# Performance work log

Hardware: AMD Instinct MI355X
Metric: run time of the kernel (lower is better)

Reference implementation:

```python
import jax, jax.numpy as jnp
import numpy as np

N_NODES = 50000
N_EDGES = 800000
ENT_DIM = 128
REL_DIM = 128
NUM_REL = 200  # relation table has 2*NUM_REL rows (forward + inverse)


def setup_inputs() -> dict:
    key = jax.random.key(0)
    ks = jax.random.split(key, 16)
    inp = {
        'src': jax.random.randint(ks[0], (N_EDGES,), 0, N_NODES),
        'dst': jax.random.randint(ks[1], (N_EDGES,), 0, N_NODES),
        'etypes': jax.random.randint(ks[2], (N_EDGES,), 0, 2 * NUM_REL),
        'ent_emb': jax.random.normal(ks[3], (N_NODES, ENT_DIM), jnp.float32),
        'rel_emb': jax.random.normal(ks[4], (2 * NUM_REL, REL_DIM), jnp.float32),
        'W_O_w': jax.random.normal(ks[5], (ENT_DIM, REL_DIM + ENT_DIM), jnp.float32) * 0.05,
        'W_O_b': jax.random.normal(ks[6], (ENT_DIM,), jnp.float32) * 0.05,
        'W_I_w': jax.random.normal(ks[7], (ENT_DIM, REL_DIM + ENT_DIM), jnp.float32) * 0.05,
        'W_I_b': jax.random.normal(ks[8], (ENT_DIM,), jnp.float32) * 0.05,
        'W_S_w': jax.random.normal(ks[9], (ENT_DIM, ENT_DIM), jnp.float32) * 0.05,
        'W_S_b': jax.random.normal(ks[10], (ENT_DIM,), jnp.float32) * 0.05,
        'W_R_w': jax.random.normal(ks[11], (REL_DIM, REL_DIM), jnp.float32) * 0.05,
        'W_R_b': jax.random.normal(ks[12], (REL_DIM,), jnp.float32) * 0.05,
    }
    return inp


def reference(src, dst, etypes, ent_emb, rel_emb,
              W_O_w, W_O_b, W_I_w, W_I_b, W_S_w, W_S_b, W_R_w, W_R_b):
    # msg_func: per-edge gather of relation emb and source node emb, concat,
    # then route through W_O (type < num_rel) or W_I (type >= num_rel).
    comp_h = jnp.concatenate([rel_emb[etypes], ent_emb[src]], axis=-1)  # [E, rel+ent]
    msg_o = comp_h @ W_O_w.T + W_O_b  # [E, ent]
    msg_i = comp_h @ W_I_w.T + W_I_b
    non_inv = (etypes < NUM_REL)[:, None]
    msg = jnp.where(non_inv, msg_o, msg_i)
    # fn.mean('msg','h_agg'): scatter-mean into destination nodes (0 if no in-edges)
    agg_sum = jax.ops.segment_sum(msg, dst, num_segments=N_NODES)
    deg = jax.ops.segment_sum(jnp.ones((msg.shape[0],), msg.dtype), dst,
                              num_segments=N_NODES)
    h_agg = agg_sum / jnp.maximum(deg, 1.0)[:, None]
    # apply_node_func (act is None -> identity)
    ent_new = ent_emb @ W_S_w.T + W_S_b + h_agg
    # edge_update
    rel_new = rel_emb @ W_R_w.T + W_R_b
    return ent_new, rel_new
```

## Files before the change

kernel.cpp:

```cpp
#include <hip/hip_runtime.h>
#include <hip/hip_bf16.h>

#define N_NODES 50000
#define N_EDGES 800000
#define DIM 128
#define NUM_REL 200
#define NREL2 (2 * NUM_REL)
#define NROWG (N_NODES / 16)
#define NBLK_G ((NROWG + 3) / 4)
#define NODES_PER_XCD (N_NODES / 8)
#define CAP 64
#define ZROW (2 * N_NODES)
#define ZREL NREL2
#define ZPAY (ZROW | (ZREL << 17))

typedef __bf16 bf16x8 __attribute__((ext_vector_type(8)));
typedef float f32x4 __attribute__((ext_vector_type(4)));

__global__ void __launch_bounds__(256)
prep_kernel(const float* __restrict__ W_O_w, const float* __restrict__ W_I_w,
            const float* __restrict__ W_S_w,
            __bf16* __restrict__ WTh, __bf16* __restrict__ WTl,
            int* __restrict__ counts, __bf16* __restrict__ EEb,
            __bf16* __restrict__ Rb) {
    const int idx = blockIdx.x * 256 + threadIdx.x;
    if (idx < 384 * DIM) {
        const int j = idx >> 7;
        const int k = idx & 127;
        float v;
        if (j < 128) v = W_O_w[j * (2 * DIM) + DIM + k];
        else if (j < 256) v = W_I_w[(j - 128) * (2 * DIM) + DIM + k];
        else v = W_S_w[(j - 256) * DIM + k];
        const __bf16 h = (__bf16)v;
        WTh[idx] = h;
        WTl[idx] = (__bf16)(v - (float)h);
    }
    if (idx < N_NODES) counts[idx] = 0;
    if (idx < DIM) {
        EEb[(size_t)ZROW * DIM + idx] = (__bf16)0.f;
        Rb[(size_t)ZREL * DIM + idx] = (__bf16)0.f;
    }
}

__global__ void rel_tables_kernel(const float* __restrict__ rel_emb,
                                  const float* __restrict__ W_O_w,
                                  const float* __restrict__ W_O_b,
                                  const float* __restrict__ W_I_w,
                                  const float* __restrict__ W_I_b,
                                  const float* __restrict__ W_R_w,
                                  const float* __restrict__ W_R_b,
                                  __bf16* __restrict__ Rb,
                                  float* __restrict__ rel_new) {
    __shared__ float row[DIM];
    const int t = blockIdx.x;
    const int j = threadIdx.x;
    row[j] = rel_emb[t * DIM + j];
    __syncthreads();

    const bool fwd = (t < NUM_REL);
    const float* __restrict__ wSel = (fwd ? W_O_w : W_I_w) + j * (2 * DIM);
    const float* __restrict__ wR = W_R_w + j * DIM;

    float aSel = 0.f, aR = 0.f;
#pragma unroll 8
    for (int k = 0; k < DIM; ++k) {
        const float e = row[k];
        aSel += e * wSel[k];
        aR += e * wR[k];
    }
    Rb[t * DIM + j] = (__bf16)(aSel + (fwd ? W_O_b[j] : W_I_b[j]));
    rel_new[t * DIM + j] = aR + W_R_b[j];
}

#define REP4(F) F(0) F(1) F(2) F(3)

__global__ void __launch_bounds__(256, 1)
mfma_gemm_kernel(const float* __restrict__ ent,
                 const __bf16* __restrict__ WTh, const __bf16* __restrict__ WTl,
                 const float* __restrict__ W_S_b,
                 __bf16* __restrict__ EEb, float* __restrict__ ent_S) {
    __shared__ __bf16 LBh[2][16 * 64 * 8];
    __shared__ __bf16 LBl[2][16 * 64 * 8];

    const int tid = threadIdx.x;
    const int wv = tid >> 6;
    const int rg = blockIdx.x * 4 + wv;
    const bool valid = (rg < NROWG);
    const int rgc = valid ? rg : (NROWG - 1);
    const int l = tid & 63;
    const int r16 = l & 15;
    const int kg = l >> 4;

    const float* __restrict__ aptr = ent + (size_t)(rgc * 16 + r16) * DIM + kg * 8;
#define ADECL(ks)                                                              \
    bf16x8 ah##ks, al##ks;                                                     \
    {                                                                          \
        const float4 v0 = *(const float4*)(aptr + (ks) * 32);                  \
        const float4 v1 = *(const float4*)(aptr + (ks) * 32 + 4);              \
        const float xs[8] = {v0.x, v0.y, v0.z, v0.w, v1.x, v1.y, v1.z, v1.w};  \
        _Pragma("unroll") for (int i = 0; i < 8; ++i) {                        \
            const __bf16 h = (__bf16)xs[i];                                    \
            ah##ks[i] = h;                                                     \
            al##ks[i] = (__bf16)(xs[i] - (float)h);                            \
        }                                                                      \
    }
    REP4(ADECL)
#undef ADECL

    const int orow = rgc * 16 + kg * 4;

#pragma unroll
    for (int i = 0; i < 4; ++i) {
        const int sks = i * 4 + wv;
        const int s = sks >> 2;
        const int ks = sks & 3;
        const size_t soff = (size_t)(s * 16 + r16) * DIM + ks * 32 + kg * 8;
        const int g = i * 256 + tid;
        *(bf16x8*)(&LBh[0][g * 8]) = *(const bf16x8*)(WTh + soff);
        *(bf16x8*)(&LBl[0][g * 8]) = *(const bf16x8*)(WTl + soff);
    }

#pragma unroll 1
    for (int cb = 0; cb < 6; ++cb) {
        __syncthreads();
        const int cur = cb & 1;
        const int nxt = cur ^ 1;

        bf16x8 ph0, ph1, ph2, ph3, pl0, pl1, pl2, pl3;
        if (cb < 5) {
            const int cbn = cb + 1;
#define PRE(i)                                                                 \
            {                                                                  \
                const int sks = (i) * 4 + wv;                                  \
                const int s = sks >> 2;                                        \
                const int ks = sks & 3;                                        \
                const size_t soff =                                            \
                    (size_t)(cbn * 64 + s * 16 + r16) * DIM + ks * 32 + kg * 8;\
                ph##i = *(const bf16x8*)(WTh + soff);                          \
                pl##i = *(const bf16x8*)(WTl + soff);                          \
            }
            PRE(0) PRE(1) PRE(2) PRE(3)
#undef PRE
        }

        f32x4 p0 = {0.f, 0.f, 0.f, 0.f}, q0 = {0.f, 0.f, 0.f, 0.f};
        f32x4 p1 = {0.f, 0.f, 0.f, 0.f}, q1 = {0.f, 0.f, 0.f, 0.f};
        f32x4 p2 = {0.f, 0.f, 0.f, 0.f}, q2 = {0.f, 0.f, 0.f, 0.f};
        f32x4 p3 = {0.f, 0.f, 0.f, 0.f}, q3 = {0.f, 0.f, 0.f, 0.f};

#define KS(ks)                                                                 \
    {                                                                          \
        const bf16x8 bh0 = *(const bf16x8*)(&LBh[cur][((0 * 4 + (ks)) * 64 + l) * 8]); \
        const bf16x8 bh1 = *(const bf16x8*)(&LBh[cur][((1 * 4 + (ks)) * 64 + l) * 8]); \
        const bf16x8 bh2 = *(const bf16x8*)(&LBh[cur][((2 * 4 + (ks)) * 64 + l) * 8]); \
        const bf16x8 bh3 = *(const bf16x8*)(&LBh[cur][((3 * 4 + (ks)) * 64 + l) * 8]); \
        const bf16x8 bl0 = *(const bf16x8*)(&LBl[cur][((0 * 4 + (ks)) * 64 + l) * 8]); \
        const bf16x8 bl1 = *(const bf16x8*)(&LBl[cur][((1 * 4 + (ks)) * 64 + l) * 8]); \
        const bf16x8 bl2 = *(const bf16x8*)(&LBl[cur][((2 * 4 + (ks)) * 64 + l) * 8]); \
        const bf16x8 bl3 = *(const bf16x8*)(&LBl[cur][((3 * 4 + (ks)) * 64 + l) * 8]); \
        p0 = __builtin_amdgcn_mfma_f32_16x16x32_bf16(ah##ks, bh0, p0, 0, 0, 0); \
        p1 = __builtin_amdgcn_mfma_f32_16x16x32_bf16(ah##ks, bh1, p1, 0, 0, 0); \
        p2 = __builtin_amdgcn_mfma_f32_16x16x32_bf16(ah##ks, bh2, p2, 0, 0, 0); \
        p3 = __builtin_amdgcn_mfma_f32_16x16x32_bf16(ah##ks, bh3, p3, 0, 0, 0); \
        q0 = __builtin_amdgcn_mfma_f32_16x16x32_bf16(al##ks, bh0, q0, 0, 0, 0); \
        q1 = __builtin_amdgcn_mfma_f32_16x16x32_bf16(al##ks, bh1, q1, 0, 0, 0); \
        q2 = __builtin_amdgcn_mfma_f32_16x16x32_bf16(al##ks, bh2, q2, 0, 0, 0); \
        q3 = __builtin_amdgcn_mfma_f32_16x16x32_bf16(al##ks, bh3, q3, 0, 0, 0); \
        q0 = __builtin_amdgcn_mfma_f32_16x16x32_bf16(ah##ks, bl0, q0, 0, 0, 0); \
        q1 = __builtin_amdgcn_mfma_f32_16x16x32_bf16(ah##ks, bl1, q1, 0, 0, 0); \
        q2 = __builtin_amdgcn_mfma_f32_16x16x32_bf16(ah##ks, bl2, q2, 0, 0, 0); \
        q3 = __builtin_amdgcn_mfma_f32_16x16x32_bf16(ah##ks, bl3, q3, 0, 0, 0); \
    }
        REP4(KS)
#undef KS

        if (cb < 5) {
#define WRT(i)                                                                 \
            {                                                                  \
                const int g = (i) * 256 + tid;                                 \
                *(bf16x8*)(&LBh[nxt][g * 8]) = ph##i;                          \
                *(bf16x8*)(&LBl[nxt][g * 8]) = pl##i;                          \
            }
            WRT(0) WRT(1) WRT(2) WRT(3)
#undef WRT
        }

        if (valid) {
            const int colb = (cb & 1) * 64;
            if (cb < 4) {
                __bf16* __restrict__ obb =
                    EEb + ((cb < 2) ? 0 : (size_t)N_NODES * DIM);
#define ST(s, P, Q)                                                            \
                {                                                              \
                    const int col = colb + (s) * 16 + r16;                     \
                    const f32x4 a = P + Q;                                     \
                    obb[(size_t)(orow + 0) * DIM + col] = (__bf16)a[0];        \
                    obb[(size_t)(orow + 1) * DIM + col] = (__bf16)a[1];        \
                    obb[(size_t)(orow + 2) * DIM + col] = (__bf16)a[2];        \
                    obb[(size_t)(orow + 3) * DIM + col] = (__bf16)a[3];        \
                }
                ST(0, p0, q0) ST(1, p1, q1) ST(2, p2, q2) ST(3, p3, q3)
#undef ST
            } else {
#define ST(s, P, Q)                                                            \
                {                                                              \
                    const int col = colb + (s) * 16 + r16;                     \
                    const float bs = W_S_b[col];                               \
                    const f32x4 a = P + Q;                                     \
                    ent_S[(size_t)(orow + 0) * DIM + col] = a[0] + bs;         \
                    ent_S[(size_t)(orow + 1) * DIM + col] = a[1] + bs;         \
                    ent_S[(size_t)(orow + 2) * DIM + col] = a[2] + bs;         \
                    ent_S[(size_t)(orow + 3) * DIM + col] = a[3] + bs;         \
                }
                ST(0, p0, q0) ST(1, p1, q1) ST(2, p2, q2) ST(3, p3, q3)
#undef ST
            }
        }
    }
}

__global__ void __launch_bounds__(256)
fill_kernel(const int* __restrict__ src, const int* __restrict__ dst,
            const int* __restrict__ et, int* __restrict__ counts,
            int* __restrict__ sp) {
    const int b = blockIdx.x;
    const int r = b & 7;
    const int e = (b >> 3) * 256 + threadIdx.x;
    const int d = dst[e];
    if ((unsigned)(d - r * NODES_PER_XCD) < (unsigned)NODES_PER_XCD) {
        const int t = et[e];
        const int row = src[e] + ((t < NUM_REL) ? 0 : N_NODES);
        const int pos = atomicAdd(&counts[d], 1);
        if (pos < CAP) sp[(d << 6) + pos] = row | (t << 17);
    }
}

__global__ void __launch_bounds__(256)
gather_kernel(const int* __restrict__ counts, const int* __restrict__ sp,
              const __bf16* __restrict__ EEb, const __bf16* __restrict__ Rb,
              const float* __restrict__ ent_S, float* __restrict__ out_ent) {
    const int node = blockIdx.x * 4 + (threadIdx.x >> 6);
    if (node >= N_NODES) return;
    const int l = threadIdx.x & 63;
    const int q = l >> 4;
    const int m = l & 15;

    const int cntT = counts[node];
    const int cnt = min(cntT, CAP);

    float a0 = 0.f, a1 = 0.f, a2 = 0.f, a3 = 0.f;
    float a4 = 0.f, a5 = 0.f, a6 = 0.f, a7 = 0.f;
    const char* __restrict__ Eb = (const char*)EEb + 16 * m;
    const char* __restrict__ Rp = (const char*)Rb + 16 * m;

    const int myp = (l < cnt) ? sp[(node << 6) + l] : ZPAY;
#pragma unroll 2
    for (int i = 0; i < cnt; i += 4) {
        const int p = __shfl(myp, i + q);
        const unsigned eoff = (unsigned)(p & 0x1FFFF) << 8;
        const unsigned roff = ((unsigned)p >> 17) << 8;
        const uint4 ev = *(const uint4*)(Eb + eoff);
        const uint4 rv = *(const uint4*)(Rp + roff);
        a0 += __uint_as_float(ev.x << 16) + __uint_as_float(rv.x << 16);
        a1 += __uint_as_float(ev.x & 0xffff0000u) +
              __uint_as_float(rv.x & 0xffff0000u);
        a2 += __uint_as_float(ev.y << 16) + __uint_as_float(rv.y << 16);
        a3 += __uint_as_float(ev.y & 0xffff0000u) +
              __uint_as_float(rv.y & 0xffff0000u);
        a4 += __uint_as_float(ev.z << 16) + __uint_as_float(rv.z << 16);
        a5 += __uint_as_float(ev.z & 0xffff0000u) +
              __uint_as_float(rv.z & 0xffff0000u);
        a6 += __uint_as_float(ev.w << 16) + __uint_as_float(rv.w << 16);
        a7 += __uint_as_float(ev.w & 0xffff0000u) +
              __uint_as_float(rv.w & 0xffff0000u);
    }

#define RED(A) A += __shfl_xor(A, 16); A += __shfl_xor(A, 32);
    RED(a0) RED(a1) RED(a2) RED(a3) RED(a4) RED(a5) RED(a6) RED(a7)
#undef RED

    if (l < 16) {
        const float inv = 1.0f / fmaxf((float)cntT, 1.0f);
        const float* sp_ = ent_S + (size_t)node * DIM + 8 * m;
        const float4 s0 = *(const float4*)(sp_);
        const float4 s1 = *(const float4*)(sp_ + 4);
        float4 o0, o1;
        o0.x = s0.x + a0 * inv;
        o0.y = s0.y + a1 * inv;
        o0.z = s0.z + a2 * inv;
        o0.w = s0.w + a3 * inv;
        o1.x = s1.x + a4 * inv;
        o1.y = s1.y + a5 * inv;
        o1.z = s1.z + a6 * inv;
        o1.w = s1.w + a7 * inv;
        float* op = out_ent + (size_t)node * DIM + 8 * m;
        *(float4*)(op) = o0;
        *(float4*)(op + 4) = o1;
    }
}

extern "C" void kernel_launch(void* const* d_in, const int* in_sizes, int n_in,
                              void* d_out, int out_size, void* d_ws, size_t ws_size,
                              hipStream_t stream) {
    const int* src = (const int*)d_in[0];
    const int* dst = (const int*)d_in[1];
    const int* et = (const int*)d_in[2];
    const float* ent_emb = (const float*)d_in[3];
    const float* rel_emb = (const float*)d_in[4];
    const float* W_O_w = (const float*)d_in[5];
    const float* W_O_b = (const float*)d_in[6];
    const float* W_I_w = (const float*)d_in[7];
    const float* W_I_b = (const float*)d_in[8];
    const float* W_S_w = (const float*)d_in[9];
    const float* W_S_b = (const float*)d_in[10];
    const float* W_R_w = (const float*)d_in[11];
    const float* W_R_b = (const float*)d_in[12];

    float* out_ent = (float*)d_out;
    float* out_rel = out_ent + (size_t)N_NODES * DIM;

    float* wsf = (float*)d_ws;
    float* ent_S = wsf;
    wsf += (size_t)N_NODES * DIM;
    __bf16* EEb = (__bf16*)wsf;
    wsf += ((size_t)(2 * N_NODES + 1) * DIM + 1) / 2;
    __bf16* Rb = (__bf16*)wsf;
    wsf += (size_t)(NREL2 + 1) * DIM / 2;
    __bf16* WTh = (__bf16*)wsf;
    wsf += 384 * DIM / 2;
    __bf16* WTl = (__bf16*)wsf;
    wsf += 384 * DIM / 2;
    int* counts = (int*)wsf;
    int* sp = counts + N_NODES;

    prep_kernel<<<(N_NODES + 255) / 256, 256, 0, stream>>>(
        W_O_w, W_I_w, W_S_w, WTh, WTl, counts, EEb, Rb);

    rel_tables_kernel<<<NREL2, DIM, 0, stream>>>(rel_emb, W_O_w, W_O_b, W_I_w, W_I_b,
                                                 W_R_w, W_R_b, Rb, out_rel);

    mfma_gemm_kernel<<<NBLK_G, 256, 0, stream>>>(
        ent_emb, WTh, WTl, W_S_b, EEb, ent_S);

    fill_kernel<<<(N_EDGES / 256) * 8, 256, 0, stream>>>(src, dst, et, counts, sp);

    gather_kernel<<<(N_NODES + 3) / 4, 256, 0, stream>>>(counts, sp, EEb, Rb,
                                                         ent_S, out_ent);
}
```

Before: 131.9 us.

## Fuse edge fill into GEMM launch and merge prep with relation tables

Merges the weight-prep and relation-table kernels into one launch, and appends edge-bucketing fill blocks to the GEMM grid so the atomics-heavy fill overlaps with the MFMA work. This cuts launches from five to three and lets otherwise idle CUs work during the GEMM. The GEMM's shared-memory double buffering is removed in favour of a single buffer with two barriers per stage. That halves LDS use, which helps fill blocks co-reside, but exposes the weight-load latency.

```diff
diff --git a/kernel.cpp b/kernel.cpp
--- a/kernel.cpp
+++ b/kernel.cpp
@@ -8,6 +8,8 @@
 #define NREL2 (2 * NUM_REL)
 #define NROWG (N_NODES / 16)
 #define NBLK_G ((NROWG + 3) / 4)
+#define FILL_NB 2048
+#define NCHUNK_E (N_EDGES / 256)
 #define NODES_PER_XCD (N_NODES / 8)
 #define CAP 64
 #define ZROW (2 * N_NODES)
@@ -18,69 +20,85 @@
 typedef float f32x4 __attribute__((ext_vector_type(4)));
 
 __global__ void __launch_bounds__(256)
-prep_kernel(const float* __restrict__ W_O_w, const float* __restrict__ W_I_w,
-            const float* __restrict__ W_S_w,
-            __bf16* __restrict__ WTh, __bf16* __restrict__ WTl,
-            int* __restrict__ counts, __bf16* __restrict__ EEb,
-            __bf16* __restrict__ Rb) {
-    const int idx = blockIdx.x * 256 + threadIdx.x;
-    if (idx < 384 * DIM) {
-        const int j = idx >> 7;
-        const int k = idx & 127;
-        float v;
-        if (j < 128) v = W_O_w[j * (2 * DIM) + DIM + k];
-        else if (j < 256) v = W_I_w[(j - 128) * (2 * DIM) + DIM + k];
-        else v = W_S_w[(j - 256) * DIM + k];
-        const __bf16 h = (__bf16)v;
-        WTh[idx] = h;
-        WTl[idx] = (__bf16)(v - (float)h);
-    }
-    if (idx < N_NODES) counts[idx] = 0;
-    if (idx < DIM) {
-        EEb[(size_t)ZROW * DIM + idx] = (__bf16)0.f;
-        Rb[(size_t)ZREL * DIM + idx] = (__bf16)0.f;
+prep_rel_kernel(const float* __restrict__ rel_emb,
+                const float* __restrict__ W_O_w, const float* __restrict__ W_O_b,
+                const float* __restrict__ W_I_w, const float* __restrict__ W_I_b,
+                const float* __restrict__ W_R_w, const float* __restrict__ W_R_b,
+                const float* __restrict__ W_S_w,
+                __bf16* __restrict__ WTh, __bf16* __restrict__ WTl,
+                int* __restrict__ counts, __bf16* __restrict__ EEb,
+                __bf16* __restrict__ Rb, float* __restrict__ rel_new) {
+    const int bid = blockIdx.x;
+    if (bid < NREL2 / 2) {
+        __shared__ float row[2][DIM];
+        const int h = threadIdx.x >> 7;
+        const int j = threadIdx.x & 127;
+        const int t = bid * 2 + h;
+        row[h][j] = rel_emb[t * DIM + j];
+        __syncthreads();
+
+        const bool fwd = (t < NUM_REL);
+        const float* __restrict__ wSel = (fwd ? W_O_w : W_I_w) + j * (2 * DIM);
+        const float* __restrict__ wR = W_R_w + j * DIM;
+        float aSel = 0.f, aR = 0.f;
+#pragma unroll 8
+        for (int k = 0; k < DIM; ++k) {
+            const float e = row[h][k];
+            aSel += e * wSel[k];
+            aR += e * wR[k];
+        }
+        Rb[t * DIM + j] = (__bf16)(aSel + (fwd ? W_O_b[j] : W_I_b[j]));
+        rel_new[t * DIM + j] = aR + W_R_b[j];
+    } else {
+        const int idx = (bid - NREL2 / 2) * 256 + threadIdx.x;
+        if (idx < 384 * DIM) {
+            const int j = idx >> 7;
+            const int k = idx & 127;
+            float v;
+            if (j < 128) v = W_O_w[j * (2 * DIM) + DIM + k];
+            else if (j < 256) v = W_I_w[(j - 128) * (2 * DIM) + DIM + k];
+            else v = W_S_w[(j - 256) * DIM + k];
+            const __bf16 h = (__bf16)v;
+            WTh[idx] = h;
+            WTl[idx] = (__bf16)(v - (float)h);
+        }
+        if (idx < N_NODES) counts[idx] = 0;
+        if (idx < DIM) {
+            EEb[(size_t)ZROW * DIM + idx] = (__bf16)0.f;
+            Rb[(size_t)ZREL * DIM + idx] = (__bf16)0.f;
+        }
     }
 }
 
-__global__ void rel_tables_kernel(const float* __restrict__ rel_emb,
-                                  const float* __restrict__ W_O_w,
-                                  const float* __restrict__ W_O_b,
-                                  const float* __restrict__ W_I_w,
-                                  const float* __restrict__ W_I_b,
-                                  const float* __restrict__ W_R_w,
-                                  const float* __restrict__ W_R_b,
-                                  __bf16* __restrict__ Rb,
-                                  float* __restrict__ rel_new) {
-    __shared__ float row[DIM];
-    const int t = blockIdx.x;
-    const int j = threadIdx.x;
-    row[j] = rel_emb[t * DIM + j];
-    __syncthreads();
-
-    const bool fwd = (t < NUM_REL);
-    const float* __restrict__ wSel = (fwd ? W_O_w : W_I_w) + j * (2 * DIM);
-    const float* __restrict__ wR = W_R_w + j * DIM;
-
-    float aSel = 0.f, aR = 0.f;
-#pragma unroll 8
-    for (int k = 0; k < DIM; ++k) {
-        const float e = row[k];
-        aSel += e * wSel[k];
-        aR += e * wR[k];
-    }
-    Rb[t * DIM + j] = (__bf16)(aSel + (fwd ? W_O_b[j] : W_I_b[j]));
-    rel_new[t * DIM + j] = aR + W_R_b[j];
-}
-
 #define REP4(F) F(0) F(1) F(2) F(3)
 
 __global__ void __launch_bounds__(256, 1)
-mfma_gemm_kernel(const float* __restrict__ ent,
+gemm_fill_kernel(const float* __restrict__ ent,
                  const __bf16* __restrict__ WTh, const __bf16* __restrict__ WTl,
                  const float* __restrict__ W_S_b,
-                 __bf16* __restrict__ EEb, float* __restrict__ ent_S) {
-    __shared__ __bf16 LBh[2][16 * 64 * 8];
-    __shared__ __bf16 LBl[2][16 * 64 * 8];
+                 __bf16* __restrict__ EEb, float* __restrict__ ent_S,
+                 const int* __restrict__ src, const int* __restrict__ dst,
+                 const int* __restrict__ et, int* __restrict__ counts,
+                 int* __restrict__ sp) {
+    __shared__ __bf16 LBh[16 * 64 * 8];
+    __shared__ __bf16 LBl[16 * 64 * 8];
+
+    if (blockIdx.x >= NBLK_G) {
+        const int fb = blockIdx.x - NBLK_G;
+        const int r = blockIdx.x & 7;
+#pragma unroll 1
+        for (int c = fb >> 3; c < NCHUNK_E; c += FILL_NB / 8) {
+            const int e = c * 256 + threadIdx.x;
+            const int d = dst[e];
+            if ((unsigned)(d - r * NODES_PER_XCD) < (unsigned)NODES_PER_XCD) {
+                const int t = et[e];
+                const int row = src[e] + ((t < NUM_REL) ? 0 : N_NODES);
+                const int pos = atomicAdd(&counts[d], 1);
+                if (pos < CAP) sp[(d << 6) + pos] = row | (t << 17);
+            }
+        }
+        return;
+    }
 
     const int tid = threadIdx.x;
     const int wv = tid >> 6;
@@ -109,39 +127,21 @@
 
     const int orow = rgc * 16 + kg * 4;
 
-#pragma unroll
-    for (int i = 0; i < 4; ++i) {
-        const int sks = i * 4 + wv;
-        const int s = sks >> 2;
-        const int ks = sks & 3;
-        const size_t soff = (size_t)(s * 16 + r16) * DIM + ks * 32 + kg * 8;
-        const int g = i * 256 + tid;
-        *(bf16x8*)(&LBh[0][g * 8]) = *(const bf16x8*)(WTh + soff);
-        *(bf16x8*)(&LBl[0][g * 8]) = *(const bf16x8*)(WTl + soff);
-    }
-
 #pragma unroll 1
     for (int cb = 0; cb < 6; ++cb) {
         __syncthreads();
-        const int cur = cb & 1;
-        const int nxt = cur ^ 1;
-
-        bf16x8 ph0, ph1, ph2, ph3, pl0, pl1, pl2, pl3;
-        if (cb < 5) {
-            const int cbn = cb + 1;
-#define PRE(i)                                                                 \
-            {                                                                  \
-                const int sks = (i) * 4 + wv;                                  \
-                const int s = sks >> 2;                                        \
-                const int ks = sks & 3;                                        \
-                const size_t soff =                                            \
-                    (size_t)(cbn * 64 + s * 16 + r16) * DIM + ks * 32 + kg * 8;\
-                ph##i = *(const bf16x8*)(WTh + soff);                          \
-                pl##i = *(const bf16x8*)(WTl + soff);                          \
-            }
-            PRE(0) PRE(1) PRE(2) PRE(3)
-#undef PRE
-        }
+#pragma unroll
+        for (int i = 0; i < 4; ++i) {
+            const int sks = i * 4 + wv;
+            const int s = sks >> 2;
+            const int ks = sks & 3;
+            const size_t soff =
+                (size_t)(cb * 64 + s * 16 + r16) * DIM + ks * 32 + kg * 8;
+            const int g = i * 256 + tid;
+            *(bf16x8*)(&LBh[g * 8]) = *(const bf16x8*)(WTh + soff);
+            *(bf16x8*)(&LBl[g * 8]) = *(const bf16x8*)(WTl + soff);
+        }
+        __syncthreads();
 
         f32x4 p0 = {0.f, 0.f, 0.f, 0.f}, q0 = {0.f, 0.f, 0.f, 0.f};
         f32x4 p1 = {0.f, 0.f, 0.f, 0.f}, q1 = {0.f, 0.f, 0.f, 0.f};
@@ -150,14 +150,14 @@
 
 #define KS(ks)                                                                 \
     {                                                                          \
-        const bf16x8 bh0 = *(const bf16x8*)(&LBh[cur][((0 * 4 + (ks)) * 64 + l) * 8]); \
-        const bf16x8 bh1 = *(const bf16x8*)(&LBh[cur][((1 * 4 + (ks)) * 64 + l) * 8]); \
-        const bf16x8 bh2 = *(const bf16x8*)(&LBh[cur][((2 * 4 + (ks)) * 64 + l) * 8]); \
-        const bf16x8 bh3 = *(const bf16x8*)(&LBh[cur][((3 * 4 + (ks)) * 64 + l) * 8]); \
-        const bf16x8 bl0 = *(const bf16x8*)(&LBl[cur][((0 * 4 + (ks)) * 64 + l) * 8]); \
-        const bf16x8 bl1 = *(const bf16x8*)(&LBl[cur][((1 * 4 + (ks)) * 64 + l) * 8]); \
-        const bf16x8 bl2 = *(const bf16x8*)(&LBl[cur][((2 * 4 + (ks)) * 64 + l) * 8]); \
-        const bf16x8 bl3 = *(const bf16x8*)(&LBl[cur][((3 * 4 + (ks)) * 64 + l) * 8]); \
+        const bf16x8 bh0 = *(const bf16x8*)(&LBh[((0 * 4 + (ks)) * 64 + l) * 8]); \
+        const bf16x8 bh1 = *(const bf16x8*)(&LBh[((1 * 4 + (ks)) * 64 + l) * 8]); \
+        const bf16x8 bh2 = *(const bf16x8*)(&LBh[((2 * 4 + (ks)) * 64 + l) * 8]); \
+        const bf16x8 bh3 = *(const bf16x8*)(&LBh[((3 * 4 + (ks)) * 64 + l) * 8]); \
+        const bf16x8 bl0 = *(const bf16x8*)(&LBl[((0 * 4 + (ks)) * 64 + l) * 8]); \
+        const bf16x8 bl1 = *(const bf16x8*)(&LBl[((1 * 4 + (ks)) * 64 + l) * 8]); \
+        const bf16x8 bl2 = *(const bf16x8*)(&LBl[((2 * 4 + (ks)) * 64 + l) * 8]); \
+        const bf16x8 bl3 = *(const bf16x8*)(&LBl[((3 * 4 + (ks)) * 64 + l) * 8]); \
         p0 = __builtin_amdgcn_mfma_f32_16x16x32_bf16(ah##ks, bh0, p0, 0, 0, 0); \
         p1 = __builtin_amdgcn_mfma_f32_16x16x32_bf16(ah##ks, bh1, p1, 0, 0, 0); \
         p2 = __builtin_amdgcn_mfma_f32_16x16x32_bf16(ah##ks, bh2, p2, 0, 0, 0); \
@@ -173,17 +173,6 @@
     }
         REP4(KS)
 #undef KS
-
-        if (cb < 5) {
-#define WRT(i)                                                                 \
-            {                                                                  \
-                const int g = (i) * 256 + tid;                                 \
-                *(bf16x8*)(&LBh[nxt][g * 8]) = ph##i;                          \
-                *(bf16x8*)(&LBl[nxt][g * 8]) = pl##i;                          \
-            }
-            WRT(0) WRT(1) WRT(2) WRT(3)
-#undef WRT
-        }
 
         if (valid) {
             const int colb = (cb & 1) * 64;
@@ -220,22 +209,6 @@
 }
 
 __global__ void __launch_bounds__(256)
-fill_kernel(const int* __restrict__ src, const int* __restrict__ dst,
-            const int* __restrict__ et, int* __restrict__ counts,
-            int* __restrict__ sp) {
-    const int b = blockIdx.x;
-    const int r = b & 7;
-    const int e = (b >> 3) * 256 + threadIdx.x;
-    const int d = dst[e];
-    if ((unsigned)(d - r * NODES_PER_XCD) < (unsigned)NODES_PER_XCD) {
-        const int t = et[e];
-        const int row = src[e] + ((t < NUM_REL) ? 0 : N_NODES);
-        const int pos = atomicAdd(&counts[d], 1);
-        if (pos < CAP) sp[(d << 6) + pos] = row | (t << 17);
-    }
-}
-
-__global__ void __launch_bounds__(256)
 gather_kernel(const int* __restrict__ counts, const int* __restrict__ sp,
               const __bf16* __restrict__ EEb, const __bf16* __restrict__ Rb,
               const float* __restrict__ ent_S, float* __restrict__ out_ent) {
@@ -333,16 +306,12 @@
     int* counts = (int*)wsf;
     int* sp = counts + N_NODES;
 
-    prep_kernel<<<(N_NODES + 255) / 256, 256, 0, stream>>>(
-        W_O_w, W_I_w, W_S_w, WTh, WTl, counts, EEb, Rb);
-
-    rel_tables_kernel<<<NREL2, DIM, 0, stream>>>(rel_emb, W_O_w, W_O_b, W_I_w, W_I_b,
-                                                 W_R_w, W_R_b, Rb, out_rel);
-
-    mfma_gemm_kernel<<<NBLK_G, 256, 0, stream>>>(
-        ent_emb, WTh, WTl, W_S_b, EEb, ent_S);
-
-    fill_kernel<<<(N_EDGES / 256) * 8, 256, 0, stream>>>(src, dst, et, counts, sp);
+    prep_rel_kernel<<<NREL2 / 2 + 196, 256, 0, stream>>>(
+        rel_emb, W_O_w, W_O_b, W_I_w, W_I_b, W_R_w, W_R_b, W_S_w,
+        WTh, WTl, counts, EEb, Rb, out_rel);
+
+    gemm_fill_kernel<<<NBLK_G + FILL_NB, 256, 0, stream>>>(
+        ent_emb, WTh, WTl, W_S_b, EEb, ent_S, src, dst, et, counts, sp);
 
     gather_kernel<<<(N_NODES + 3) / 4, 256, 0, stream>>>(counts, sp, EEb, Rb,
                                                          ent_S, out_ent);
```

Result: faster. 121.1 us (-8.2%).
